# Performance work log

Hardware: AMD Instinct MI355X
Metric: run time of the kernel (lower is better)

The kernel has to match this reference:

```python
import jax, jax.numpy as jnp
import numpy as np

OUT_F, IN_F = 4096, 4096
TOKENS = 8192


def setup_inputs() -> dict:
    key = jax.random.key(0)
    k0, k1, k2, k3 = jax.random.split(key, 4)
    CORE_SCALE = 0.05  # keep reconstructed W finite and well below the 1e6 sanity bound
    x = jax.random.normal(k0, (TOKENS, IN_F), dtype=jnp.float32)
    core0 = jax.random.normal(k1, (1, 16, 16, 64), dtype=jnp.float32) * CORE_SCALE
    core1 = jax.random.normal(k2, (64, 16, 16, 64), dtype=jnp.float32) * CORE_SCALE
    core2 = jax.random.normal(k3, (64, 16, 16, 1), dtype=jnp.float32) * CORE_SCALE
    return {"x": x, "core0": core0, "core1": core1, "core2": core2}


def _build_weight(cores):
    # Chain tensordot over bond dims: cores[k] is [r_{k-1}, o_k, i_k, r_k]
    t = cores[0].astype(jnp.float32)
    for c in cores[1:]:
        t = jnp.tensordot(t, c.astype(jnp.float32), axes=((-1,), (0,)))
    # squeeze the boundary bonds (both 1 for open boundary)
    t = t[0, ..., 0]  # shape [o1, i1, o2, i2, o3, i3]
    num = len(cores)
    # order 'oi': all o-axes first, then all i-axes (matches _contract_4d_chain_with)
    perm = list(range(0, 2 * num, 2)) + list(range(1, 2 * num, 2))
    t = jnp.transpose(t, perm)
    W = t.reshape(OUT_F, IN_F)
    # _clean_finite: nan/inf -> 0 (identity on finite values)
    return jnp.nan_to_num(W, nan=0.0, posinf=0.0, neginf=0.0)


def reference(x, core0, core1, core2):
    W = _build_weight([core0, core1, core2])  # [out_f, in_f], fp32
    # dense path: y = x @ W^T (nn.Linear semantics, no bias)
    return jnp.matmul(x, W.T)
```

## Files before the change

### kernel.cpp

```cpp
#include <hip/hip_runtime.h>

typedef __attribute__((ext_vector_type(8))) short  s8v;
typedef __attribute__((ext_vector_type(8))) unsigned short us8;
typedef __attribute__((ext_vector_type(4))) unsigned short us4;
typedef __attribute__((ext_vector_type(4))) float  f4v;

__device__ __forceinline__ unsigned short f2bf(float f) {
  unsigned int u = __builtin_bit_cast(unsigned int, f);
  u += 0x7fffu + ((u >> 16) & 1u);
  return (unsigned short)(u >> 16);
}

__device__ __forceinline__ void gll16(const void* g, void* l) {
  __builtin_amdgcn_global_load_lds(
      (const __attribute__((address_space(1))) unsigned int*)g,
      (__attribute__((address_space(3))) unsigned int*)l, 16, 0, 0);
}

__global__ __launch_bounds__(256) void cast_bf16(const float* __restrict__ in,
                                                 unsigned short* __restrict__ out) {
  const size_t i = (size_t)blockIdx.x * 256 + threadIdx.x;
  const f4v* p = (const f4v*)in;
  f4v a = p[2 * i];
  f4v b = p[2 * i + 1];
  us8 r;
  r[0] = f2bf(a[0]); r[1] = f2bf(a[1]); r[2] = f2bf(a[2]); r[3] = f2bf(a[3]);
  r[4] = f2bf(b[0]); r[5] = f2bf(b[1]); r[6] = f2bf(b[2]); r[7] = f2bf(b[3]);
  *(us8*)&out[i * 8] = r;
}

__global__ __launch_bounds__(256) void contract1b(const float* __restrict__ c0,
                                                  const float* __restrict__ c1,
                                                  unsigned short* __restrict__ T) {
  const int idx = blockIdx.x * 256 + threadIdx.x;
  const int r2q = idx & 15;
  const int oi2 = (idx >> 4) & 255;
  const int oi1 = idx >> 12;
  const float* c0p = c0 + oi1 * 64;
  const float* c1p = c1 + oi2 * 64 + r2q * 4;
  f4v s = (f4v)0.f;
#pragma unroll 8
  for (int r1 = 0; r1 < 64; ++r1) {
    const float t = c0p[r1];
    const f4v v = *(const f4v*)(c1p + r1 * 16384);
    s[0] = fmaf(t, v[0], s[0]); s[1] = fmaf(t, v[1], s[1]);
    s[2] = fmaf(t, v[2], s[2]); s[3] = fmaf(t, v[3], s[3]);
  }
  us4 o;
  o[0] = f2bf(s[0]); o[1] = f2bf(s[1]); o[2] = f2bf(s[2]); o[3] = f2bf(s[3]);
  *(us4*)&T[(size_t)idx * 4] = o;
}

__global__ __launch_bounds__(256) void transc2(const float* __restrict__ c2,
                                               unsigned short* __restrict__ c2t) {
  const int n = blockIdx.x * 16 + (threadIdx.x >> 4);
  const int j = threadIdx.x & 15;
  us4 o;
#pragma unroll
  for (int q = 0; q < 4; ++q) o[q] = f2bf(c2[(j * 4 + q) * 256 + n]);
  *(us4*)&c2t[(size_t)n * 64 + j * 4] = o;
}

__global__ __launch_bounds__(256) void buildW3(const unsigned short* __restrict__ T,
                                               const unsigned short* __restrict__ c2t,
                                               unsigned short* __restrict__ W) {
  __shared__ unsigned short sT[16384];
  __shared__ unsigned short sC[16384];

  const int tid = threadIdx.x;
  const int o1 = blockIdx.x >> 4, o2 = blockIdx.x & 15;

#pragma unroll
  for (int j = 0; j < 8; ++j) {
    const int c = j * 256 + tid;
    const int m = c >> 3, sl = c & 7;
    const int dst = m * 64 + ((sl ^ (m & 7)) << 3);
    *(us8*)&sT[dst] = *(const us8*)(T + (size_t)(o1 * 16 + (m >> 4)) * 16384 +
                                    (o2 * 16 + (m & 15)) * 64 + sl * 8);
    *(us8*)&sC[dst] = *(const us8*)(c2t + (size_t)m * 64 + sl * 8);
  }
  __syncthreads();

  const int lane = tid & 63, wid = tid >> 6;
  const int fr = lane & 15, ks = lane >> 4;
  const int f7 = fr & 7;
  const int sx0 = ((ks ^ f7) << 3);
  const int sx1 = (((4 + ks) ^ f7) << 3);

  s8v a[4][2];
#pragma unroll
  for (int mi = 0; mi < 4; ++mi) {
    const unsigned short* p = &sT[(wid * 64 + mi * 16 + fr) * 64];
    a[mi][0] = *(const s8v*)(p + sx0);
    a[mi][1] = *(const s8v*)(p + sx1);
  }
#pragma unroll
  for (int nt = 0; nt < 16; ++nt) {
    const unsigned short* p = &sC[(nt * 16 + fr) * 64];
    const s8v b0 = *(const s8v*)(p + sx0);
    const s8v b1 = *(const s8v*)(p + sx1);
#pragma unroll
    for (int mi = 0; mi < 4; ++mi) {
      f4v acc = (f4v)0.f;
      acc = __builtin_amdgcn_mfma_f32_16x16x32_bf16(a[mi][0], b0, acc, 0, 0, 0);
      acc = __builtin_amdgcn_mfma_f32_16x16x32_bf16(a[mi][1], b1, acc, 0, 0, 0);
      unsigned short* wp = W + (size_t)(o1 * 256 + o2 * 16 + nt) * 4096 +
                           (wid * 4 + mi) * 256 + fr;
#pragma unroll
      for (int r = 0; r < 4; ++r) wp[(ks * 4 + r) * 16] = f2bf(acc[r]);
    }
  }
}


#define BAR() __builtin_amdgcn_s_barrier()
#define VMW(N) asm volatile("s_waitcnt vmcnt(" #N ")" ::: "memory")

template<int MQ, int NQ>
__device__ __forceinline__ void mmq(f4v (&acc)[8][4], const s8v (&a)[4][2], const s8v (&b)[2][2]) {
  __builtin_amdgcn_s_setprio(1);
#pragma unroll
  for (int mi = 0; mi < 4; ++mi)
#pragma unroll
    for (int ni = 0; ni < 2; ++ni)
#pragma unroll
      for (int q = 0; q < 2; ++q)
        acc[MQ * 4 + mi][NQ * 2 + ni] = __builtin_amdgcn_mfma_f32_16x16x32_bf16(
            a[mi][q], b[ni][q], acc[MQ * 4 + mi][NQ * 2 + ni], 0, 0, 0);
  __builtin_amdgcn_s_setprio(0);
}

__global__ __launch_bounds__(512, 2) void gemm8(const unsigned short* __restrict__ A,
                                                const unsigned short* __restrict__ B,
                                                float* __restrict__ C) {
  constexpr int N = 4096, K = 4096;
  constexpr int NT = K / 64;
  constexpr int NITER = NT / 2;
  constexpr int NXT = N / 256;

  __shared__ unsigned short lds[65536];

  const int tid  = threadIdx.x;
  const int lane = tid & 63;
  const int wid  = tid >> 6;
  const int wm   = wid >> 2;
  const int wn   = wid & 3;

  const int cpx = (int)gridDim.x >> 3;
  const int wg  = ((int)blockIdx.x & 7) * cpx + ((int)blockIdx.x >> 3);
  const long bm = (long)(wg / NXT) * 256;
  const long bn = (long)(wg % NXT) * 256;

  const int srow = tid >> 3;
  const int scol = ((tid & 7) ^ (srow & 7)) * 8;
  const unsigned short* gA = A + (bm + srow) * (size_t)K + scol;
  const unsigned short* gB = B + (bn + srow) * (size_t)K + scol;
  const size_t half64 = 64 * (size_t)K;
  const size_t k128   = 128 * (size_t)K;

#define STG(gp, koff, ldsU) do {                                  \
    const unsigned short* g_ = (gp) + (koff);                     \
    gll16(g_,          &lds[(ldsU) + tid * 8]);                   \
    gll16(g_ + half64, &lds[(ldsU) + 4096 + tid * 8]);            \
  } while (0)

  const int fr = lane & 15;
  const int ks = lane >> 4;
  const int f7 = fr & 7;
  const int sx0 = (ks ^ f7) * 8;
  const int sx1 = ((ks | 4) ^ f7) * 8;
  const int arow = (wm * 64 + fr) * 64;
  const int brow = (wn * 32 + fr) * 64;

#define RDA(dst, MQ, bufU) do {                                              \
    const unsigned short* p_ = &lds[(bufU) + (MQ) * 8192 + arow];            \
    dst[0][0] = *(const s8v*)(p_ + sx0);        dst[0][1] = *(const s8v*)(p_ + sx1); \
    dst[1][0] = *(const s8v*)(p_ + 1024 + sx0); dst[1][1] = *(const s8v*)(p_ + 1024 + sx1); \
    dst[2][0] = *(const s8v*)(p_ + 2048 + sx0); dst[2][1] = *(const s8v*)(p_ + 2048 + sx1); \
    dst[3][0] = *(const s8v*)(p_ + 3072 + sx0); dst[3][1] = *(const s8v*)(p_ + 3072 + sx1); \
  } while (0)
#define RDB(dst, NQ, bufU) do {                                              \
    const unsigned short* p_ = &lds[(bufU) + 16384 + (NQ) * 8192 + brow];    \
    dst[0][0] = *(const s8v*)(p_ + sx0);        dst[0][1] = *(const s8v*)(p_ + sx1); \
    dst[1][0] = *(const s8v*)(p_ + 1024 + sx0); dst[1][1] = *(const s8v*)(p_ + 1024 + sx1); \
  } while (0)

  f4v acc[8][4];
#pragma unroll
  for (int m = 0; m < 8; ++m)
#pragma unroll
    for (int n = 0; n < 4; ++n) acc[m][n] = (f4v)0.0f;

  STG(gA,        0, 0);
  STG(gA + k128, 0, 8192);
  STG(gB,        0, 16384);
  STG(gB + k128, 0, 24576);
  STG(gA,        64, 32768);
  STG(gB,        64, 32768 + 16384);
  STG(gA + k128, 64, 32768 + 8192);
  VMW(6);
  BAR();

  s8v a0[4][2], a1[4][2], b0[2][2], b1[2][2];
  RDA(a0, 0, 0);
  RDB(b0, 0, 0);

  for (int i = 0; i < NITER; ++i) {
    const long w2 = (i == NITER - 1) ? -128L : 0L;
    const long w3 = (i == NITER - 1) ? -192L : 0L;
    RDB(b1, 1, 0);
    STG(gB + k128, 64, 32768 + 24576);
    mmq<0, 0>(acc, a0, b0);
    BAR();
    RDA(a1, 1, 0);
    STG(gA, 128 + w2, 0);
    mmq<0, 1>(acc, a0, b1);
    BAR();
    STG(gB, 128 + w2, 16384);
    mmq<1, 0>(acc, a1, b0);
    VMW(4); BAR();
    RDA(a0, 0, 32768);
    RDB(b0, 0, 32768);
    STG(gA + k128, 128 + w2, 8192);
    mmq<1, 1>(acc, a1, b1);
    BAR();
    RDB(b1, 1, 32768);
    STG(gB + k128, 128 + w2, 24576);
    mmq<0, 0>(acc, a0, b0);
    BAR();
    RDA(a1, 1, 32768);
    STG(gA, 192 + w3, 32768);
    mmq<0, 1>(acc, a0, b1);
    BAR();
    STG(gB, 192 + w3, 32768 + 16384);
    mmq<1, 0>(acc, a1, b0);
    VMW(4); BAR();
    RDA(a0, 0, 0);
    RDB(b0, 0, 0);
    STG(gA + k128, 192 + w3, 32768 + 8192);
    mmq<1, 1>(acc, a1, b1);
    BAR();

    gA += 128; gB += 128;
  }
  VMW(0);

#pragma unroll
  for (int mq = 0; mq < 2; ++mq)
#pragma unroll
    for (int mi = 0; mi < 4; ++mi)
#pragma unroll
      for (int nq = 0; nq < 2; ++nq)
#pragma unroll
        for (int ni = 0; ni < 2; ++ni) {
          const size_t row0 = bm + mq * 128 + wm * 64 + mi * 16 + ks * 4;
          const size_t col  = bn + nq * 128 + wn * 32 + ni * 16 + fr;
          float* cp = C + row0 * (size_t)N + col;
          f4v v = acc[mq * 4 + mi][nq * 2 + ni];
          cp[0] = v[0]; cp[N] = v[1]; cp[2 * (size_t)N] = v[2]; cp[3 * (size_t)N] = v[3];
        }
#undef STG
#undef RDA
#undef RDB
}

extern "C" void kernel_launch(void* const* d_in, const int* in_sizes, int n_in,
                              void* d_out, int out_size, void* d_ws, size_t ws_size,
                              hipStream_t stream) {
  const float* x  = (const float*)d_in[0];
  const float* c0 = (const float*)d_in[1];
  const float* c1 = (const float*)d_in[2];
  const float* c2 = (const float*)d_in[3];
  float* out = (float*)d_out;

  char* ws = (char*)d_ws;
  unsigned short* T   = (unsigned short*)ws;
  unsigned short* c2t = (unsigned short*)(ws + (8u << 20));
  unsigned short* Wb  = (unsigned short*)(ws + (16u << 20));
  unsigned short* xb  = (unsigned short*)(ws + (48u << 20));

  hipLaunchKernelGGL(cast_bf16,  dim3(16384), dim3(256), 0, stream, x, xb);
  hipLaunchKernelGGL(contract1b, dim3(4096),  dim3(256), 0, stream, c0, c1, T);
  hipLaunchKernelGGL(transc2,    dim3(16),    dim3(256), 0, stream, c2, c2t);
  hipLaunchKernelGGL(buildW3,    dim3(256),   dim3(256), 0, stream, T, c2t, Wb);
  hipLaunchKernelGGL(gemm8,      dim3(512),   dim3(512), 0, stream, xb, Wb, out);
}
```

Measured before the change: 325.2 us.

## Restructure GEMM main loop schedule of LDS reads, global stages and barriers

Reorders the double-buffered main loop of the bf16 GEMM so each half-iteration loads all A0/B0/B1 fragments up front, then issues global-to-LDS stages interleaved with barrier-separated MFMA quadrants. The wait count changes and the barrier macro gains compiler memory fences to prevent reordering around s_barrier. The aim is better overlap of global loads with compute and fewer pipeline stalls, at the risk of more register pressure from holding more fragments and possible LDS hazards in the new ordering.

```diff
diff --git a/kernel.cpp b/kernel.cpp
--- a/kernel.cpp
+++ b/kernel.cpp
@@ -113,7 +113,7 @@
 }
 
 
-#define BAR() __builtin_amdgcn_s_barrier()
+#define SBAR() do { asm volatile("" ::: "memory"); __builtin_amdgcn_s_barrier(); asm volatile("" ::: "memory"); } while (0)
 #define VMW(N) asm volatile("s_waitcnt vmcnt(" #N ")" ::: "memory")
 
 template<int MQ, int NQ>
@@ -197,49 +197,37 @@
   STG(gB + k128, 0, 24576);
   STG(gA,        64, 32768);
   STG(gB,        64, 32768 + 16384);
-  STG(gA + k128, 64, 32768 + 8192);
+  STG(gB + k128, 64, 32768 + 24576);
   VMW(6);
-  BAR();
+  SBAR();
 
   s8v a0[4][2], a1[4][2], b0[2][2], b1[2][2];
-  RDA(a0, 0, 0);
-  RDB(b0, 0, 0);
 
   for (int i = 0; i < NITER; ++i) {
     const long w2 = (i == NITER - 1) ? -128L : 0L;
     const long w3 = (i == NITER - 1) ? -192L : 0L;
-    RDB(b1, 1, 0);
-    STG(gB + k128, 64, 32768 + 24576);
-    mmq<0, 0>(acc, a0, b0);
-    BAR();
+    RDA(a0, 0, 0); RDB(b0, 0, 0); RDB(b1, 1, 0);
+    STG(gA + k128, 64, 32768 + 8192);
+    SBAR(); mmq<0, 0>(acc, a0, b0);
+    SBAR(); mmq<0, 1>(acc, a0, b1);
     RDA(a1, 1, 0);
     STG(gA, 128 + w2, 0);
-    mmq<0, 1>(acc, a0, b1);
-    BAR();
     STG(gB, 128 + w2, 16384);
-    mmq<1, 0>(acc, a1, b0);
-    VMW(4); BAR();
-    RDA(a0, 0, 32768);
-    RDB(b0, 0, 32768);
+    SBAR(); mmq<1, 0>(acc, a1, b0);
+    STG(gB + k128, 128 + w2, 24576);
+    SBAR(); mmq<1, 1>(acc, a1, b1);
+    VMW(6); SBAR();
+    RDA(a0, 0, 32768); RDB(b0, 0, 32768); RDB(b1, 1, 32768);
     STG(gA + k128, 128 + w2, 8192);
-    mmq<1, 1>(acc, a1, b1);
-    BAR();
-    RDB(b1, 1, 32768);
-    STG(gB + k128, 128 + w2, 24576);
-    mmq<0, 0>(acc, a0, b0);
-    BAR();
+    SBAR(); mmq<0, 0>(acc, a0, b0);
+    SBAR(); mmq<0, 1>(acc, a0, b1);
     RDA(a1, 1, 32768);
     STG(gA, 192 + w3, 32768);
-    mmq<0, 1>(acc, a0, b1);
-    BAR();
     STG(gB, 192 + w3, 32768 + 16384);
-    mmq<1, 0>(acc, a1, b0);
-    VMW(4); BAR();
-    RDA(a0, 0, 0);
-    RDB(b0, 0, 0);
-    STG(gA + k128, 192 + w3, 32768 + 8192);
-    mmq<1, 1>(acc, a1, b1);
-    BAR();
+    SBAR(); mmq<1, 0>(acc, a1, b0);
+    STG(gB + k128, 192 + w3, 32768 + 24576);
+    SBAR(); mmq<1, 1>(acc, a1, b1);
+    VMW(6); SBAR();
 
     gA += 128; gB += 128;
   }
```

Result: faster. 308.2 us (-5.2%).
